# Kernel tuning notes

Measured on AMD Instinct MI355X. Metric: run time of the kernel, lower is better.

Reference implementation:

```python
import jax, jax.numpy as jnp
import numpy as np

BLOCK = 100  # hard-coded block size in the original module


def setup_inputs() -> dict:
    key = jax.random.key(0)
    k1, k2 = jax.random.split(key)
    N_freqs = 128
    n = N_freqs * BLOCK  # 12800
    # DPP kernel: symmetric PD so every 100x100 diagonal block has positive logdet
    R = jax.random.normal(k1, (n, n), dtype=jnp.float32) * 0.05
    L_kernel = (R + R.T) * 0.5 + 2.0 * jnp.eye(n, dtype=jnp.float32)
    weights = jax.random.normal(k2, (n,), dtype=jnp.float32)
    return {"weights": weights, "L_kernel": L_kernel, "N_freqs": N_freqs}


def reference(weights, L_kernel, N_freqs):
    # Gather the N_freqs diagonal 100x100 blocks without touching off-diagonals
    blocks4 = L_kernel.reshape(N_freqs, BLOCK, N_freqs, BLOCK)
    idx = jnp.arange(N_freqs)
    diag_blocks = blocks4[idx, :, idx, :]  # [N_freqs, 100, 100]
    s = jax.nn.sigmoid(weights).reshape(N_freqs, BLOCK)  # [N_freqs, 100]
    I = jnp.eye(BLOCK, dtype=L_kernel.dtype)
    # diag(s_i) @ (B_i - I) + I, batched over blocks
    M = s[:, :, None] * (diag_blocks - I) + I  # [N_freqs, 100, 100]
    sign, logabs = jnp.linalg.slogdet(M)
    # torch.logdet returns nan for non-positive determinant
    logdets = jnp.where(sign > 0, logabs, jnp.nan)
    within_freq_dets = jnp.sum(logdets)
    within_freq_dets_tensor = logdets.astype(jnp.float32)
    return (within_freq_dets, within_freq_dets_tensor)
```

## Files before the change

kernel.cpp:

```cpp
#include <hip/hip_runtime.h>
#include <math.h>

#define BLK 100
#define NF  128
#define NTOT (NF * BLK)
#define P   104
#define NT  512

__device__ __forceinline__ float4 fnma4(float4 v, float s, const float4 p) {
    v.x -= s * p.x; v.y -= s * p.y; v.z -= s * p.z; v.w -= s * p.w; return v;
}
__device__ __forceinline__ float4 mul4(float4 v, float s) {
    v.x *= s; v.y *= s; v.z *= s; v.w *= s; return v;
}

#define LD4(r, c4) (*reinterpret_cast<float4*>(&a[(r) * P + 4 * (c4)]))

__global__ __launch_bounds__(NT) void lu_logdet_kernel(const float* __restrict__ w,
                                                       const float* __restrict__ L,
                                                       float* __restrict__ out) {
    __shared__ float a[BLK * P];

    const int f   = blockIdx.x;
    const int tid = threadIdx.x;
    const int sid = tid >> 5;
    const int g   = tid & 31;
    const int gg  = (g < 25) ? g : 24;

    const float* base = L + (size_t)f * BLK * NTOT + (size_t)f * BLK;
    for (int q = tid; q < BLK * 25; q += NT) {
        const int r  = q / 25;
        const int c0 = (q - r * 25) * 4;
        const float4 v = *reinterpret_cast<const float4*>(base + (size_t)r * NTOT + c0);
        const float sv = 1.0f / (1.0f + expf(-w[f * BLK + r]));
        const float ds = 1.0f - sv;
        float4 m;
        m.x = sv * v.x + ((c0 + 0) == r ? ds : 0.0f);
        m.y = sv * v.y + ((c0 + 1) == r ? ds : 0.0f);
        m.z = sv * v.z + ((c0 + 2) == r ? ds : 0.0f);
        m.w = sv * v.w + ((c0 + 3) == r ? ds : 0.0f);
        *reinterpret_cast<float4*>(&a[r * P + c0]) = m;
    }
    __syncthreads();

    float mant = 1.0f;
    int   e2   = 0;
    int   lneg = 0;

    for (int k0 = 0; k0 < BLK; k0 += 4) {
        const int gp = k0 >> 2;

        float4 pp0 = LD4(k0 + 0, gp);
        float4 pp1 = LD4(k0 + 1, gp);
        float4 pp2 = LD4(k0 + 2, gp);
        float4 pp3 = LD4(k0 + 3, gp);
        float4 P0  = LD4(k0 + 0, gg);
        float4 P1  = LD4(k0 + 1, gg);
        float4 P2  = LD4(k0 + 2, gg);
        float4 P3  = LD4(k0 + 3, gg);

        const float d0 = pp0.x, r0i = 1.0f / d0;
        float l;
        l = pp1.x * r0i;  pp1 = fnma4(pp1, l, pp0);  P1 = fnma4(P1, l, P0);
        const float d1 = pp1.y, r1i = 1.0f / d1;
        l = pp2.x * r0i;  pp2 = fnma4(pp2, l, pp0);  P2 = fnma4(P2, l, P0);
        l = pp2.y * r1i;  pp2 = fnma4(pp2, l, pp1);  P2 = fnma4(P2, l, P1);
        const float d2 = pp2.z, r2i = 1.0f / d2;
        l = pp3.x * r0i;  pp3 = fnma4(pp3, l, pp0);  P3 = fnma4(P3, l, P0);
        l = pp3.y * r1i;  pp3 = fnma4(pp3, l, pp1);  P3 = fnma4(P3, l, P1);
        l = pp3.z * r2i;  pp3 = fnma4(pp3, l, pp2);  P3 = fnma4(P3, l, P2);
        const float d3 = pp3.w, r3i = 1.0f / d3;

        const float4 Q3 = mul4(P3, r3i);
        const float4 Q2 = mul4(fnma4(P2, pp2.w, Q3), r2i);
        const float4 Q1 = mul4(fnma4(fnma4(P1, pp1.z, Q2), pp1.w, Q3), r1i);
        const float4 Q0 = mul4(fnma4(fnma4(fnma4(P0, pp0.y, Q1), pp0.z, Q2), pp0.w, Q3), r0i);

        mant *= d0 * d1 * d2 * d3;
        { int t; mant = frexpf(mant, &t); e2 += t; }
        lneg += (d0 < 0.0f) + (d1 < 0.0f) + (d2 < 0.0f) + (d3 < 0.0f);

        if (g > gp && g < 25) {
            int i = k0 + 4 + sid;
            for (; i + 16 < BLK; i += 32) {
                const int i2 = i + 16;
                const float4 panA = LD4(i,  gp);
                const float4 panB = LD4(i2, gp);
                float4 vA = LD4(i,  g);
                float4 vB = LD4(i2, g);
                vA = fnma4(vA, panA.x, Q0); vA = fnma4(vA, panA.y, Q1);
                vA = fnma4(vA, panA.z, Q2); vA = fnma4(vA, panA.w, Q3);
                vB = fnma4(vB, panB.x, Q0); vB = fnma4(vB, panB.y, Q1);
                vB = fnma4(vB, panB.z, Q2); vB = fnma4(vB, panB.w, Q3);
                LD4(i,  g) = vA;
                LD4(i2, g) = vB;
            }
            for (; i < BLK; i += 16) {
                const float4 pan = LD4(i, gp);
                float4 v = LD4(i, g);
                v = fnma4(v, pan.x, Q0); v = fnma4(v, pan.y, Q1);
                v = fnma4(v, pan.z, Q2); v = fnma4(v, pan.w, Q3);
                LD4(i, g) = v;
            }
        }
        __syncthreads();
    }

    if (tid == 0) {
        float ld = logf(mant) + (float)e2 * 0.69314718055994531f;
        if ((lneg & 1) || !isfinite(ld)) ld = __int_as_float(0x7fc00000);
        out[1 + f] = ld;
        atomicAdd(out, ld);
    }
}

extern "C" void kernel_launch(void* const* d_in, const int* in_sizes, int n_in,
                              void* d_out, int out_size, void* d_ws, size_t ws_size,
                              hipStream_t stream) {
    const float* w = (const float*)d_in[0];
    const float* L = (const float*)d_in[1];
    float* out = (float*)d_out;
    hipMemsetAsync(d_out, 0, sizeof(float), stream);
    lu_logdet_kernel<<<NF, NT, 0, stream>>>(w, L, out);
}
```

Baseline: 36.53 us.

## Pipeline next panel factorization on a dedicated wave with lookahead

Wave 0 updates only the next four rows, then factors the next 4-row panel while running at raised priority, and publishes its Q coefficients through a double-buffered shared array. The remaining waves read Q from that buffer and update the rest of the trailing rows. This takes the serial panel factorization off the critical path of each iteration, at the cost of extra shared-memory traffic and some load imbalance between wave 0 and the other waves.

```diff
diff --git a/kernel.cpp b/kernel.cpp
--- a/kernel.cpp
+++ b/kernel.cpp
@@ -16,16 +16,48 @@
 
 #define LD4(r, c4) (*reinterpret_cast<float4*>(&a[(r) * P + 4 * (c4)]))
 
+#define PANEL_Q(kb, gq)                                                        \
+    {                                                                          \
+        float4 pp0 = LD4((kb) + 0, (gq));                                      \
+        float4 pp1 = LD4((kb) + 1, (gq));                                      \
+        float4 pp2 = LD4((kb) + 2, (gq));                                      \
+        float4 pp3 = LD4((kb) + 3, (gq));                                      \
+        float4 P0  = LD4((kb) + 0, gg);                                        \
+        float4 P1  = LD4((kb) + 1, gg);                                        \
+        float4 P2  = LD4((kb) + 2, gg);                                        \
+        float4 P3  = LD4((kb) + 3, gg);                                        \
+        const float d0 = pp0.x, r0i = 1.0f / d0;                               \
+        float l;                                                               \
+        l = pp1.x * r0i;  pp1 = fnma4(pp1, l, pp0);  P1 = fnma4(P1, l, P0);    \
+        const float d1 = pp1.y, r1i = 1.0f / d1;                               \
+        l = pp2.x * r0i;  pp2 = fnma4(pp2, l, pp0);  P2 = fnma4(P2, l, P0);    \
+        l = pp2.y * r1i;  pp2 = fnma4(pp2, l, pp1);  P2 = fnma4(P2, l, P1);    \
+        const float d2 = pp2.z, r2i = 1.0f / d2;                               \
+        l = pp3.x * r0i;  pp3 = fnma4(pp3, l, pp0);  P3 = fnma4(P3, l, P0);    \
+        l = pp3.y * r1i;  pp3 = fnma4(pp3, l, pp1);  P3 = fnma4(P3, l, P1);    \
+        l = pp3.z * r2i;  pp3 = fnma4(pp3, l, pp2);  P3 = fnma4(P3, l, P2);    \
+        const float d3 = pp3.w, r3i = 1.0f / d3;                               \
+        Q3 = mul4(P3, r3i);                                                    \
+        Q2 = mul4(fnma4(P2, pp2.w, Q3), r2i);                                  \
+        Q1 = mul4(fnma4(fnma4(P1, pp1.z, Q2), pp1.w, Q3), r1i);                \
+        Q0 = mul4(fnma4(fnma4(fnma4(P0, pp0.y, Q1), pp0.z, Q2), pp0.w, Q3), r0i); \
+        mant *= d0 * d1 * d2 * d3;                                             \
+        { int t_; mant = frexpf(mant, &t_); e2 += t_; }                        \
+        lneg += (d0 < 0.0f) + (d1 < 0.0f) + (d2 < 0.0f) + (d3 < 0.0f);         \
+    }
+
 __global__ __launch_bounds__(NT) void lu_logdet_kernel(const float* __restrict__ w,
                                                        const float* __restrict__ L,
                                                        float* __restrict__ out) {
-    __shared__ float a[BLK * P];
+    __shared__ float  a[BLK * P];
+    __shared__ float4 qbuf[2][4][26];
 
-    const int f   = blockIdx.x;
-    const int tid = threadIdx.x;
-    const int sid = tid >> 5;
-    const int g   = tid & 31;
-    const int gg  = (g < 25) ? g : 24;
+    const int f    = blockIdx.x;
+    const int tid  = threadIdx.x;
+    const int wave = tid >> 6;
+    const int sid  = tid >> 5;
+    const int g    = tid & 31;
+    const int gg   = (g < 25) ? g : 24;
 
     const float* base = L + (size_t)f * BLK * NTOT + (size_t)f * BLK;
     for (int q = tid; q < BLK * 25; q += NT) {
@@ -46,61 +78,65 @@
     float mant = 1.0f;
     int   e2   = 0;
     int   lneg = 0;
+    float4 Q0, Q1, Q2, Q3;
 
-    for (int k0 = 0; k0 < BLK; k0 += 4) {
+    PANEL_Q(0, 0)
+
+    for (int k0 = 0; k0 <= 92; k0 += 4) {
         const int gp = k0 >> 2;
+        const int b  = gp & 1;
+        const int nb = b ^ 1;
 
-        float4 pp0 = LD4(k0 + 0, gp);
-        float4 pp1 = LD4(k0 + 1, gp);
-        float4 pp2 = LD4(k0 + 2, gp);
-        float4 pp3 = LD4(k0 + 3, gp);
-        float4 P0  = LD4(k0 + 0, gg);
-        float4 P1  = LD4(k0 + 1, gg);
-        float4 P2  = LD4(k0 + 2, gg);
-        float4 P3  = LD4(k0 + 3, gg);
-
-        const float d0 = pp0.x, r0i = 1.0f / d0;
-        float l;
-        l = pp1.x * r0i;  pp1 = fnma4(pp1, l, pp0);  P1 = fnma4(P1, l, P0);
-        const float d1 = pp1.y, r1i = 1.0f / d1;
-        l = pp2.x * r0i;  pp2 = fnma4(pp2, l, pp0);  P2 = fnma4(P2, l, P0);
-        l = pp2.y * r1i;  pp2 = fnma4(pp2, l, pp1);  P2 = fnma4(P2, l, P1);
-        const float d2 = pp2.z, r2i = 1.0f / d2;
-        l = pp3.x * r0i;  pp3 = fnma4(pp3, l, pp0);  P3 = fnma4(P3, l, P0);
-        l = pp3.y * r1i;  pp3 = fnma4(pp3, l, pp1);  P3 = fnma4(P3, l, P1);
-        l = pp3.z * r2i;  pp3 = fnma4(pp3, l, pp2);  P3 = fnma4(P3, l, P2);
-        const float d3 = pp3.w, r3i = 1.0f / d3;
-
-        const float4 Q3 = mul4(P3, r3i);
-        const float4 Q2 = mul4(fnma4(P2, pp2.w, Q3), r2i);
-        const float4 Q1 = mul4(fnma4(fnma4(P1, pp1.z, Q2), pp1.w, Q3), r1i);
-        const float4 Q0 = mul4(fnma4(fnma4(fnma4(P0, pp0.y, Q1), pp0.z, Q2), pp0.w, Q3), r0i);
-
-        mant *= d0 * d1 * d2 * d3;
-        { int t; mant = frexpf(mant, &t); e2 += t; }
-        lneg += (d0 < 0.0f) + (d1 < 0.0f) + (d2 < 0.0f) + (d3 < 0.0f);
-
-        if (g > gp && g < 25) {
-            int i = k0 + 4 + sid;
-            for (; i + 16 < BLK; i += 32) {
-                const int i2 = i + 16;
-                const float4 panA = LD4(i,  gp);
-                const float4 panB = LD4(i2, gp);
-                float4 vA = LD4(i,  g);
-                float4 vB = LD4(i2, g);
-                vA = fnma4(vA, panA.x, Q0); vA = fnma4(vA, panA.y, Q1);
-                vA = fnma4(vA, panA.z, Q2); vA = fnma4(vA, panA.w, Q3);
-                vB = fnma4(vB, panB.x, Q0); vB = fnma4(vB, panB.y, Q1);
-                vB = fnma4(vB, panB.z, Q2); vB = fnma4(vB, panB.w, Q3);
-                LD4(i,  g) = vA;
-                LD4(i2, g) = vB;
+        if (wave == 0) {
+            __builtin_amdgcn_s_setprio(1);
+            if (g > gp && g < 25) {
+                const int s  = sid & 1;
+                const int i1 = k0 + 4 + s;
+                const int i2 = k0 + 6 + s;
+                const float4 pan1 = LD4(i1, gp);
+                const float4 pan2 = LD4(i2, gp);
+                float4 v1 = LD4(i1, g);
+                float4 v2 = LD4(i2, g);
+                v1 = fnma4(v1, pan1.x, Q0); v1 = fnma4(v1, pan1.y, Q1);
+                v1 = fnma4(v1, pan1.z, Q2); v1 = fnma4(v1, pan1.w, Q3);
+                v2 = fnma4(v2, pan2.x, Q0); v2 = fnma4(v2, pan2.y, Q1);
+                v2 = fnma4(v2, pan2.z, Q2); v2 = fnma4(v2, pan2.w, Q3);
+                LD4(i1, g) = v1;
+                LD4(i2, g) = v2;
             }
-            for (; i < BLK; i += 16) {
-                const float4 pan = LD4(i, gp);
-                float4 v = LD4(i, g);
-                v = fnma4(v, pan.x, Q0); v = fnma4(v, pan.y, Q1);
-                v = fnma4(v, pan.z, Q2); v = fnma4(v, pan.w, Q3);
-                LD4(i, g) = v;
+            PANEL_Q(k0 + 4, gp + 1)
+            if (g < 25) {
+                qbuf[nb][0][g] = Q0; qbuf[nb][1][g] = Q1;
+                qbuf[nb][2][g] = Q2; qbuf[nb][3][g] = Q3;
+            }
+            __builtin_amdgcn_s_setprio(0);
+        } else {
+            if (k0 > 0) {
+                Q0 = qbuf[b][0][gg]; Q1 = qbuf[b][1][gg];
+                Q2 = qbuf[b][2][gg]; Q3 = qbuf[b][3][gg];
+            }
+            if (g > gp && g < 25) {
+                int i = k0 + 8 + (sid - 2);
+                for (; i + 14 < BLK; i += 28) {
+                    const int i2 = i + 14;
+                    const float4 panA = LD4(i,  gp);
+                    const float4 panB = LD4(i2, gp);
+                    float4 vA = LD4(i,  g);
+                    float4 vB = LD4(i2, g);
+                    vA = fnma4(vA, panA.x, Q0); vA = fnma4(vA, panA.y, Q1);
+                    vA = fnma4(vA, panA.z, Q2); vA = fnma4(vA, panA.w, Q3);
+                    vB = fnma4(vB, panB.x, Q0); vB = fnma4(vB, panB.y, Q1);
+                    vB = fnma4(vB, panB.z, Q2); vB = fnma4(vB, panB.w, Q3);
+                    LD4(i,  g) = vA;
+                    LD4(i2, g) = vB;
+                }
+                for (; i < BLK; i += 14) {
+                    const float4 pan = LD4(i, gp);
+                    float4 v = LD4(i, g);
+                    v = fnma4(v, pan.x, Q0); v = fnma4(v, pan.y, Q1);
+                    v = fnma4(v, pan.z, Q2); v = fnma4(v, pan.w, Q3);
+                    LD4(i, g) = v;
+                }
             }
         }
         __syncthreads();
```

Measured after the change: 30.43 us. 16.7% less time.
